# Kernel optimization log

Measured on AMD Instinct MI355X. Metric: run time of the kernel, lower is better.

## Reference

```python
import jax, jax.numpy as jnp
import numpy as np

# ---- static config (matches init_kwargs) ----
B, H, W = 4, 256, 256
TIN, F, P = 10, 4, 8          # time steps in, forecast steps, patch size
CIN = TIN + 2                  # x concatenated with 2-channel grid
E = 768                        # LATENT_DIMS
NB, BS = 8, 96                 # num_blocks, block_size = E // NB
HP, WP = H // P, W // P
MID = 4 * E                    # channel-mixer hidden (MLP_RATIO=4)
DEPTH = 4
LAM = 0.01                     # softshrink sparsity_threshold


def _gelu(t):
    return jax.nn.gelu(t, approximate=False)  # torch default GELU (erf)


def _shrink(t):
    return jnp.sign(t) * jnp.maximum(jnp.abs(t) - LAM, 0.0)


def _spectral(x, w1, b1, w2, b2):
    """SpectralConvBlockDiag: rfft2 -> block-diag complex MLP (GELU) -> softshrink -> irfft2 + residual."""
    bias = x
    b_, h_, w_, c_ = x.shape
    wf = w_ // 2 + 1
    xf = jnp.fft.rfft2(x, axes=(1, 2), norm='ortho').reshape(b_, h_, wf, NB, BS)
    xr, xi = jnp.real(xf), jnp.imag(xf)
    mm = lambda t, w: jnp.einsum('bhfni,nio->bhfno', t, w)
    # complex linear 1 + GELU on real/imag separately
    o1r = _gelu(mm(xr, w1[0]) - mm(xi, w1[1]) + b1[0])
    o1i = _gelu(mm(xi, w1[0]) + mm(xr, w1[1]) + b1[1])
    # complex linear 2 + softshrink
    o2r = _shrink(mm(o1r, w2[0]) - mm(o1i, w2[1]) + b2[0])
    o2i = _shrink(mm(o1i, w2[0]) + mm(o1r, w2[1]) + b2[1])
    xf = (o2r + 1j * o2i).reshape(b_, h_, wf, c_)
    out = jnp.fft.irfft2(xf, s=(h_, w_), axes=(1, 2), norm='ortho')
    return out + bias


def setup_inputs() -> dict:
    key = jax.random.key(0)
    ks = jax.random.split(key, 20)
    s = 0.02
    f32 = jnp.float32
    return {
        'x': jax.random.normal(ks[0], (B, H, W, TIN), f32),
        'grid': jax.random.uniform(ks[1], (B, H, W, 2), f32),
        'conv_w': s * jax.random.normal(ks[2], (E, CIN, P, P), f32),
        'conv_b': s * jax.random.normal(ks[3], (E,), f32),
        'pos_emb': s * jax.random.normal(ks[4], (HP, WP, E), f32),
        'w1': s * jax.random.normal(ks[5], (DEPTH, 2, NB, BS, BS), f32),
        'b1': s * jax.random.normal(ks[6], (DEPTH, 2, NB, BS), f32),
        'w2': s * jax.random.normal(ks[7], (DEPTH, 2, NB, BS, BS), f32),
        'b2': s * jax.random.normal(ks[8], (DEPTH, 2, NB, BS), f32),
        'fc1_w': s * jax.random.normal(ks[9], (DEPTH, E, MID), f32),
        'fc1_b': s * jax.random.normal(ks[10], (DEPTH, MID), f32),
        'fc2_w': s * jax.random.normal(ks[11], (DEPTH, MID, E), f32),
        'fc2_b': s * jax.random.normal(ks[12], (DEPTH, E), f32),
        'head_w1': s * jax.random.normal(ks[13], (E, 2 * E), f32),
        'head_b1': s * jax.random.normal(ks[14], (2 * E,), f32),
        'head_w2': s * jax.random.normal(ks[15], (2 * E, P * P), f32),
        'head_b2': s * jax.random.normal(ks[16], (P * P,), f32),
    }


def reference(x, grid, conv_w, conv_b, pos_emb, w1, b1, w2, b2,
              fc1_w, fc1_b, fc2_w, fc2_b, head_w1, head_b1, head_w2, head_b2):
    # concat grid channels and patch-embed (conv stride==kernel == patch einsum)
    z = jnp.concatenate([x, grid], axis=-1)                  # (B,H,W,CIN)
    patches = z.reshape(B, HP, P, WP, P, CIN)
    t = jnp.einsum('bhpwqc,ecpq->bhwe', patches, conv_w) + conv_b + pos_emb  # (B,HP,WP,E)
    states = []
    for _ in range(F):
        for d in range(DEPTH):                               # AFNOBoundariesBlock (no residual, identity norms)
            t = _spectral(t, w1[d], b1[d], w2[d], b2[d])
            t = _gelu(t @ fc1_w[d] + fc1_b[d]) @ fc2_w[d] + fc2_b[d]
        states.append(t)
    ls = jnp.stack(states, axis=1)                           # (B,F,HP,WP,E)
    h = _gelu(ls @ head_w1 + head_b1) @ head_w2 + head_b2    # (B,F,HP,WP,P*P)
    h = h.reshape(B, F, HP, WP, P, P, 1)
    h = jnp.transpose(h, (0, 6, 2, 4, 3, 5, 1)).reshape(B, 1, H, W, F)
    return jnp.squeeze(h, axis=1)                            # (B,H,W,F)
```

## Files before the change

### kernel.cpp

```cpp
#include <hip/hip_runtime.h>
#include <hip/hip_bf16.h>
#include <math.h>


typedef __attribute__((ext_vector_type(8))) _Float16 half8;
typedef __attribute__((ext_vector_type(4))) _Float16 half4v;
typedef __attribute__((ext_vector_type(4))) float float4v;

__device__ __forceinline__ float gelu_f(float v) {
    return 0.5f * v * (1.0f + erff(v * 0.70710678118654752f));
}
__device__ __forceinline__ float shrink_f(float v) {
    return (v > 0.01f) ? (v - 0.01f) : ((v < -0.01f) ? (v + 0.01f) : 0.0f);
}

#define STEP32 0.19634954084936207f

__device__ __forceinline__ void async16(const void* g, void* l) {
    __builtin_amdgcn_global_load_lds(
        (const __attribute__((address_space(1))) unsigned int*)g,
        (__attribute__((address_space(3))) unsigned int*)l, 16, 0, 0);
}

__global__ __launch_bounds__(256) void gather_patch(const float* __restrict__ x,
        const float* __restrict__ grd, _Float16* __restrict__ A)
{
    int idx = blockIdx.x * 256 + threadIdx.x;
    int j   = idx % 768;
    int tok = idx / 768;
    int c = j >> 6, p = (j >> 3) & 7, q = j & 7;
    int wp = tok & 31, hp = (tok >> 5) & 31, b = tok >> 10;
    int hh = hp * 8 + p, ww = wp * 8 + q;
    float v;
    if (c < 10) v = x[((b * 256 + hh) * 256 + ww) * 10 + c];
    else        v = grd[((b * 256 + hh) * 256 + ww) * 2 + (c - 10)];
    A[idx] = (_Float16)v;
}

__global__ __launch_bounds__(256) void dft_fwd_w(const _Float16* __restrict__ th,
        _Float16* __restrict__ Xr, _Float16* __restrict__ Xi)
{
    __shared__ float2 lut[32];
    int bh = blockIdx.x;
    int tid = threadIdx.x;
    if (tid < 32) { float a = tid * STEP32; lut[tid] = make_float2(cosf(a), sinf(a)); }
    __syncthreads();
    int b = bh >> 5, h = bh & 31;
    int c = blockIdx.y * 256 + tid;
    float v[32];
    #pragma unroll
    for (int w = 0; w < 32; ++w) v[w] = (float)th[(bh * 32 + w) * 768 + c];
    for (int kw = 0; kw <= 16; ++kw) {
        float ar = 0.f, ai = 0.f;
        #pragma unroll
        for (int w = 0; w < 32; ++w) {
            float2 cs = lut[(kw * w) & 31];
            ar += v[w] * cs.x;
            ai -= v[w] * cs.y;
        }
        size_t g = ((size_t)(b * 17 + kw) * 32 + h) * 768 + c;
        Xr[g] = (_Float16)(ar * 0.03125f);
        Xi[g] = (_Float16)(ai * 0.03125f);
    }
}

__global__ __launch_bounds__(256) void dft_inv_w(const _Float16* __restrict__ Yr,
        const _Float16* __restrict__ Yi, _Float16* __restrict__ th)
{
    __shared__ float2 lut[32];
    int bh = blockIdx.x;
    int tid = threadIdx.x;
    if (tid < 32) { float a = tid * STEP32; lut[tid] = make_float2(cosf(a), sinf(a)); }
    __syncthreads();
    int b = bh >> 5, h = bh & 31;
    int c = blockIdx.y * 256 + tid;
    float yr[17], yi[16];
    #pragma unroll
    for (int k = 0; k <= 16; ++k) yr[k] = (float)Yr[((size_t)(b * 17 + k) * 32 + h) * 768 + c];
    #pragma unroll
    for (int k = 1; k <= 15; ++k) yi[k] = (float)Yi[((size_t)(b * 17 + k) * 32 + h) * 768 + c];
    for (int w = 0; w < 32; ++w) {
        float val = yr[0] + ((w & 1) ? -yr[16] : yr[16]);
        #pragma unroll
        for (int k = 1; k <= 15; ++k) {
            float2 cs = lut[(k * w) & 31];
            val += 2.f * (yr[k] * cs.x - yi[k] * cs.y);
        }
        int gi = (bh * 32 + w) * 768 + c;
        th[gi] = (_Float16)(val * 0.03125f + (float)th[gi]);
    }
}

__global__ __launch_bounds__(256) void prep_specw(const float* __restrict__ w1,
        const float* __restrict__ w2, _Float16* __restrict__ out)
{
    __shared__ float tile[96][97];
    int mid = blockIdx.x;
    int n  = mid & 7;
    int ri = (mid >> 3) & 1;
    int l  = (mid >> 4) & 1;
    int d  = mid >> 5;
    const float* src = (l ? w2 : w1) + ((size_t)(d * 2 + ri) * 8 + n) * 9216;
    for (int idx = threadIdx.x; idx < 9216; idx += 256)
        tile[idx / 96][idx % 96] = src[idx];
    __syncthreads();
    _Float16* dst = out + (size_t)mid * 9216;
    for (int idx = threadIdx.x; idx < 9216; idx += 256)
        dst[idx] = (_Float16)tile[idx % 96][idx / 96];
}

__global__ __launch_bounds__(256) void spec_fused(
        _Float16* __restrict__ Xr, _Float16* __restrict__ Xi,
        const _Float16* __restrict__ W1r, const _Float16* __restrict__ W1i,
        const _Float16* __restrict__ W2r, const _Float16* __restrict__ W2i,
        const float* __restrict__ b1r, const float* __restrict__ b1i,
        const float* __restrict__ b2r, const float* __restrict__ b2i)
{
    __shared__ alignas(16) _Float16 Ec[1024], Es[1024];
    __shared__ alignas(16) _Float16 XTr[3840], XTi[3840];
    __shared__ alignas(16) _Float16 Zr[3328], Zi[3328];
    __shared__ alignas(16) _Float16 Sr[3328], Si[3328];

    const int bk = blockIdx.x;
    const int n  = blockIdx.y;
    const int tid = threadIdx.x;
    const int wave = tid >> 6, lane = tid & 63;
    const int wr = wave >> 1, wc = wave & 1;
    const int lr = lane & 15, quad = lane >> 4;
    const size_t base = (size_t)bk * 24576 + n * 96;

    for (int i = tid; i < 1024; i += 256) {
        int kh = i >> 5, h = i & 31;
        float a = ((kh * h) & 31) * STEP32;
        Ec[i] = (_Float16)cosf(a);
        Es[i] = (_Float16)sinf(a);
    }
    for (int i = tid; i < 384; i += 256) {
        int h = i / 12, cc = (i % 12) * 8;
        half8 vr = *(const half8*)(Xr + base + (size_t)h * 768 + cc);
        half8 vi = *(const half8*)(Xi + base + (size_t)h * 768 + cc);
        #pragma unroll
        for (int e = 0; e < 8; ++e) {
            XTr[(cc + e) * 40 + h] = vr[e];
            XTi[(cc + e) * 40 + h] = vi[e];
        }
    }
    __syncthreads();

    const _Float16* w1r = W1r + (size_t)n * 9216;
    const _Float16* w1i = W1i + (size_t)n * 9216;
    const _Float16* w2r = W2r + (size_t)n * 9216;
    const _Float16* w2i = W2i + (size_t)n * 9216;

    half8 eC = *(const half8*)&Ec[(wr * 16 + lr) * 32 + quad * 8];
    half8 eS = *(const half8*)&Es[(wr * 16 + lr) * 32 + quad * 8];
    half8 eSn = -eS;

    {
        float4v zr[3], zi[3];
        #pragma unroll
        for (int j = 0; j < 3; ++j) { float4v z = {0,0,0,0}; zr[j] = z; zi[j] = z; }
        #pragma unroll
        for (int j = 0; j < 3; ++j) {
            int c = wc * 48 + j * 16 + lr;
            half8 xr = *(const half8*)&XTr[c * 40 + quad * 8];
            half8 xi = *(const half8*)&XTi[c * 40 + quad * 8];
            zr[j] = __builtin_amdgcn_mfma_f32_16x16x32_f16(eC,  xr, zr[j], 0, 0, 0);
            zr[j] = __builtin_amdgcn_mfma_f32_16x16x32_f16(eS,  xi, zr[j], 0, 0, 0);
            zi[j] = __builtin_amdgcn_mfma_f32_16x16x32_f16(eC,  xi, zi[j], 0, 0, 0);
            zi[j] = __builtin_amdgcn_mfma_f32_16x16x32_f16(eSn, xr, zi[j], 0, 0, 0);
        }
        #pragma unroll
        for (int j = 0; j < 3; ++j) {
            int c = wc * 48 + j * 16 + lr;
            #pragma unroll
            for (int r = 0; r < 4; ++r) {
                int kh = wr * 16 + quad * 4 + r;
                Zr[kh * 104 + c] = (_Float16)zr[j][r];
                Zi[kh * 104 + c] = (_Float16)zi[j][r];
            }
        }
    }
    __syncthreads();

    {
        float4v sr[3], si[3];
        #pragma unroll
        for (int j = 0; j < 3; ++j) { float4v z = {0,0,0,0}; sr[j] = z; si[j] = z; }
        #pragma unroll
        for (int kc = 0; kc < 3; ++kc) {
            half8 ar = *(const half8*)&Zr[(wr * 16 + lr) * 104 + kc * 32 + quad * 8];
            half8 ai = *(const half8*)&Zi[(wr * 16 + lr) * 104 + kc * 32 + quad * 8];
            half8 ain = -ai;
            #pragma unroll
            for (int j = 0; j < 3; ++j) {
                int o = wc * 48 + j * 16 + lr;
                half8 br = *(const half8*)&w1r[o * 96 + kc * 32 + quad * 8];
                half8 bi = *(const half8*)&w1i[o * 96 + kc * 32 + quad * 8];
                sr[j] = __builtin_amdgcn_mfma_f32_16x16x32_f16(ar,  br, sr[j], 0, 0, 0);
                sr[j] = __builtin_amdgcn_mfma_f32_16x16x32_f16(ain, bi, sr[j], 0, 0, 0);
                si[j] = __builtin_amdgcn_mfma_f32_16x16x32_f16(ai,  br, si[j], 0, 0, 0);
                si[j] = __builtin_amdgcn_mfma_f32_16x16x32_f16(ar,  bi, si[j], 0, 0, 0);
            }
        }
        #pragma unroll
        for (int j = 0; j < 3; ++j) {
            int o = wc * 48 + j * 16 + lr;
            float br = b1r[n * 96 + o], bi = b1i[n * 96 + o];
            #pragma unroll
            for (int r = 0; r < 4; ++r) {
                int kh = wr * 16 + quad * 4 + r;
                Sr[kh * 104 + o] = (_Float16)gelu_f(sr[j][r] + br);
                Si[kh * 104 + o] = (_Float16)gelu_f(si[j][r] + bi);
            }
        }
    }
    __syncthreads();

    {
        float4v tr[3], ti[3];
        #pragma unroll
        for (int j = 0; j < 3; ++j) { float4v z = {0,0,0,0}; tr[j] = z; ti[j] = z; }
        #pragma unroll
        for (int kc = 0; kc < 3; ++kc) {
            half8 ar = *(const half8*)&Sr[(wr * 16 + lr) * 104 + kc * 32 + quad * 8];
            half8 ai = *(const half8*)&Si[(wr * 16 + lr) * 104 + kc * 32 + quad * 8];
            half8 ain = -ai;
            #pragma unroll
            for (int j = 0; j < 3; ++j) {
                int o = wc * 48 + j * 16 + lr;
                half8 br = *(const half8*)&w2r[o * 96 + kc * 32 + quad * 8];
                half8 bi = *(const half8*)&w2i[o * 96 + kc * 32 + quad * 8];
                tr[j] = __builtin_amdgcn_mfma_f32_16x16x32_f16(ar,  br, tr[j], 0, 0, 0);
                tr[j] = __builtin_amdgcn_mfma_f32_16x16x32_f16(ain, bi, tr[j], 0, 0, 0);
                ti[j] = __builtin_amdgcn_mfma_f32_16x16x32_f16(ai,  br, ti[j], 0, 0, 0);
                ti[j] = __builtin_amdgcn_mfma_f32_16x16x32_f16(ar,  bi, ti[j], 0, 0, 0);
            }
        }
        #pragma unroll
        for (int j = 0; j < 3; ++j) {
            int o = wc * 48 + j * 16 + lr;
            float br = b2r[n * 96 + o], bi = b2i[n * 96 + o];
            #pragma unroll
            for (int r = 0; r < 4; ++r) {
                int kh = wr * 16 + quad * 4 + r;
                XTr[o * 40 + kh] = (_Float16)shrink_f(tr[j][r] + br);
                XTi[o * 40 + kh] = (_Float16)shrink_f(ti[j][r] + bi);
            }
        }
    }
    __syncthreads();

    {
        float4v yr[3], yi[3];
        #pragma unroll
        for (int j = 0; j < 3; ++j) { float4v z = {0,0,0,0}; yr[j] = z; yi[j] = z; }
        #pragma unroll
        for (int j = 0; j < 3; ++j) {
            int c = wc * 48 + j * 16 + lr;
            half8 t2r = *(const half8*)&XTr[c * 40 + quad * 8];
            half8 t2i = *(const half8*)&XTi[c * 40 + quad * 8];
            yr[j] = __builtin_amdgcn_mfma_f32_16x16x32_f16(eC,  t2r, yr[j], 0, 0, 0);
            yr[j] = __builtin_amdgcn_mfma_f32_16x16x32_f16(eSn, t2i, yr[j], 0, 0, 0);
            yi[j] = __builtin_amdgcn_mfma_f32_16x16x32_f16(eC,  t2i, yi[j], 0, 0, 0);
            yi[j] = __builtin_amdgcn_mfma_f32_16x16x32_f16(eS,  t2r, yi[j], 0, 0, 0);
        }
        #pragma unroll
        for (int j = 0; j < 3; ++j) {
            int c = wc * 48 + j * 16 + lr;
            #pragma unroll
            for (int r = 0; r < 4; ++r) {
                int h = wr * 16 + quad * 4 + r;
                Zr[h * 104 + c] = (_Float16)yr[j][r];
                Zi[h * 104 + c] = (_Float16)yi[j][r];
            }
        }
    }
    __syncthreads();

    for (int i = tid; i < 384; i += 256) {
        int h = i / 12, cc = (i % 12) * 8;
        half8 vr = *(const half8*)&Zr[h * 104 + cc];
        half8 vi = *(const half8*)&Zi[h * 104 + cc];
        *(half8*)(Xr + base + (size_t)h * 768 + cc) = vr;
        *(half8*)(Xi + base + (size_t)h * 768 + cc) = vi;
    }
}

__global__ __launch_bounds__(256) void cvt_f16(const float* __restrict__ in,
        _Float16* __restrict__ out)
{
    int i = blockIdx.x * 256 + threadIdx.x;
    float4 v = ((const float4*)in)[i];
    half4v o;
    o.x = (_Float16)v.x; o.y = (_Float16)v.y; o.z = (_Float16)v.z; o.w = (_Float16)v.w;
    ((half4v*)out)[i] = o;
}

__global__ __launch_bounds__(256) void cvt_transpose(const float* __restrict__ in,
        _Float16* __restrict__ out, int K, int N)
{
    __shared__ float tile[32][33];
    int kb = blockIdx.x * 32, nb = blockIdx.y * 32;
    int tx = threadIdx.x & 31, ty = threadIdx.x >> 5;
    #pragma unroll
    for (int r = 0; r < 32; r += 8)
        tile[ty + r][tx] = in[(size_t)(kb + ty + r) * N + nb + tx];
    __syncthreads();
    #pragma unroll
    for (int r = 0; r < 32; r += 8)
        out[(size_t)(nb + ty + r) * K + kb + tx] = (_Float16)tile[tx][ty + r];
}

template<int BN, int ACT>
__global__ __launch_bounds__(512, 4) void gemm128d(const _Float16* __restrict__ A,
        const _Float16* __restrict__ Bt, const float* __restrict__ bias,
        _Float16* __restrict__ C16, int M, int N, int K)
{
    constexpr int WN  = BN / 4;
    constexpr int FN  = WN / 16;
    constexpr int AU  = 2;
    constexpr int BU  = BN / 64;
    constexpr int LPT = AU + BU;
    __shared__ _Float16 Al[2][128 * 64];
    __shared__ _Float16 Bl[2][BN * 64];

    const int tid  = threadIdx.x;
    const int wave = tid >> 6;
    const int lane = tid & 63;
    const int wr   = wave >> 2;
    const int wc   = wave & 3;
    const int lr   = lane & 15;
    const int quad = lane >> 4;

    const int gx = gridDim.x, gy = gridDim.y, nbk = gx * gy;
    int bx = blockIdx.x, by = blockIdx.y;
    if (!(gy & 3) && !(gx & 1)) {
        int id = by * gx + bx;
        int xcd = id & 7, j = id >> 3;
        int cols = gx >> 1;
        int rows = gy >> 2;
        int jr = j / cols, jc = j % cols;
        by = (xcd >> 1) * rows + jr;
        bx = (xcd & 1) * cols + jc;
    } else if (!(nbk & 7)) {
        int id  = by * gx + bx;
        int id2 = (id & 7) * (nbk >> 3) + (id >> 3);
        by = id2 / gx; bx = id2 % gx;
    }
    const int row0 = by * 128;
    const int col0 = bx * BN;

    const int srow = lane >> 3;
    const int schk = (lane & 7) ^ (srow & 7);
    const _Float16* Ab = A  + (size_t)(row0 + wave * 8 + srow) * K + schk * 8;
    const _Float16* Bb = Bt + (size_t)(col0 + wave * 8 + srow) * K + schk * 8;

    auto stage = [&](int b, int kt) {
        const int k0 = kt * 64;
        #pragma unroll
        for (int u = 0; u < AU; ++u)
            async16(Ab + (size_t)u * 64 * K + k0, &Al[b][(u * 64 + wave * 8) * 64]);
        #pragma unroll
        for (int u = 0; u < BU; ++u)
            async16(Bb + (size_t)u * 64 * K + k0, &Bl[b][(u * 64 + wave * 8) * 64]);
    };

    float4v acc[4][FN];
    #pragma unroll
    for (int m = 0; m < 4; ++m)
        #pragma unroll
        for (int n = 0; n < FN; ++n) {
            float4v z = {0.f, 0.f, 0.f, 0.f};
            acc[m][n] = z;
        }

    auto compute = [&](int cb) {
        #pragma unroll
        for (int ks = 0; ks < 2; ++ks) {
            const int cA = ((ks * 4 + quad) ^ (lr & 7)) * 8;
            half8 bf[FN];
            #pragma unroll
            for (int n = 0; n < FN; ++n)
                bf[n] = *(const half8*)&Bl[cb][(wc * WN + n * 16 + lr) * 64 + cA];
            half8 af[4];
            #pragma unroll
            for (int m = 0; m < 4; ++m)
                af[m] = *(const half8*)&Al[cb][(wr * 64 + m * 16 + lr) * 64 + cA];
            __builtin_amdgcn_s_setprio(1);
            #pragma unroll
            for (int m = 0; m < 4; ++m)
                #pragma unroll
                for (int n = 0; n < FN; ++n)
                    acc[m][n] = __builtin_amdgcn_mfma_f32_16x16x32_f16(af[m], bf[n], acc[m][n], 0, 0, 0);
            __builtin_amdgcn_s_setprio(0);
        }
    };

    const int NT = K >> 6;
    stage(0, 0);
    stage(1, 1);
    for (int t = 0; t < NT; ++t) {
        if (t + 1 < NT) asm volatile("s_waitcnt vmcnt(5)" ::: "memory");
        else            asm volatile("s_waitcnt vmcnt(0)" ::: "memory");
        __builtin_amdgcn_s_barrier();
        compute(t & 1);
        __builtin_amdgcn_s_barrier();
        if (t + 2 < NT) stage(t & 1, t + 2);
    }

    #pragma unroll
    for (int n = 0; n < FN; ++n) {
        int col = col0 + wc * WN + n * 16 + lr;
        float bj = bias[col];
        #pragma unroll
        for (int m = 0; m < 4; ++m) {
            int row = row0 + wr * 64 + m * 16 + quad * 4;
            #pragma unroll
            for (int r = 0; r < 4; ++r) {
                float v = acc[m][n][r] + bj;
                if (ACT) v = gelu_f(v);
                C16[(size_t)(row + r) * N + col] = (_Float16)v;
            }
        }
    }
}

__global__ __launch_bounds__(256, 2) void fc2_fused(const _Float16* __restrict__ A,
        const _Float16* __restrict__ Bt, const float* __restrict__ bias,
        _Float16* __restrict__ C16, _Float16* __restrict__ XR,
        _Float16* __restrict__ XI)
{
    constexpr int K = 3072;
    constexpr int NT = 48;
    __shared__ _Float16 Al[2][64 * 64];
    __shared__ _Float16 Bl[2][96 * 64];
    __shared__ alignas(16) _Float16 Tl[2 * 96 * 40];
    __shared__ alignas(16) _Float16 ECl[1024], ESl[1024];

    const int tid  = threadIdx.x;
    const int wave = tid >> 6;
    const int lane = tid & 63;
    const int wr   = wave >> 1;
    const int wc   = wave & 1;
    const int lr   = lane & 15;
    const int quad = lane >> 4;

    for (int i = tid; i < 1024; i += 256) {
        int kw = i >> 5, w = i & 31;
        float a = ((kw * w) & 31) * STEP32;
        ECl[i] = (_Float16)(cosf(a) * 0.03125f);
        ESl[i] = (_Float16)(-sinf(a) * 0.03125f);
    }

    const int gx = gridDim.x, gy = gridDim.y;
    int bx = blockIdx.x, by = blockIdx.y;
    {
        int id = by * gx + bx;
        int xcd = id & 7, j = id >> 3;
        int cols = gx >> 1;
        int rows = gy >> 2;
        int jr = j / cols, jc = j % cols;
        by = (xcd >> 1) * rows + jr;
        bx = (xcd & 1) * cols + jc;
    }
    const int row0 = by * 64;
    const int col0 = bx * 96;

    const int srow = lane >> 3;
    const int schk = (lane & 7) ^ srow;
    const _Float16* Ab = A  + (size_t)(row0 + wave * 8 + srow) * K + schk * 8;
    const _Float16* Bb = Bt + (size_t)(col0 + wave * 8 + srow) * K + schk * 8;

    auto stage = [&](int b, int kt) {
        const int k0 = kt * 64;
        #pragma unroll
        for (int u = 0; u < 2; ++u)
            async16(Ab + (size_t)u * 32 * K + k0, &Al[b][(u * 32 + wave * 8) * 64]);
        #pragma unroll
        for (int u = 0; u < 3; ++u)
            async16(Bb + (size_t)u * 32 * K + k0, &Bl[b][(u * 32 + wave * 8) * 64]);
    };

    float4v acc[2][3];
    #pragma unroll
    for (int m = 0; m < 2; ++m)
        #pragma unroll
        for (int n = 0; n < 3; ++n) {
            float4v z = {0.f, 0.f, 0.f, 0.f};
            acc[m][n] = z;
        }

    auto compute = [&](int cb) {
        #pragma unroll
        for (int ks = 0; ks < 2; ++ks) {
            const int cA = ((ks * 4 + quad) ^ (lr & 7)) * 8;
            half8 bf[3];
            #pragma unroll
            for (int n = 0; n < 3; ++n)
                bf[n] = *(const half8*)&Bl[cb][(wc * 48 + n * 16 + lr) * 64 + cA];
            half8 af[2];
            #pragma unroll
            for (int m = 0; m < 2; ++m)
                af[m] = *(const half8*)&Al[cb][(wr * 32 + m * 16 + lr) * 64 + cA];
            __builtin_amdgcn_s_setprio(1);
            #pragma unroll
            for (int m = 0; m < 2; ++m)
                #pragma unroll
                for (int n = 0; n < 3; ++n)
                    acc[m][n] = __builtin_amdgcn_mfma_f32_16x16x32_f16(af[m], bf[n], acc[m][n], 0, 0, 0);
            __builtin_amdgcn_s_setprio(0);
        }
    };

    stage(0, 0);
    stage(1, 1);
    for (int t = 0; t < NT; ++t) {
        if (t + 1 < NT) asm volatile("s_waitcnt vmcnt(5)" ::: "memory");
        else            asm volatile("s_waitcnt vmcnt(0)" ::: "memory");
        __builtin_amdgcn_s_barrier();
        compute(t & 1);
        __builtin_amdgcn_s_barrier();
        if (t + 2 < NT) stage(t & 1, t + 2);
    }

    #pragma unroll
    for (int n = 0; n < 3; ++n) {
        int cc  = wc * 48 + n * 16 + lr;
        int col = col0 + cc;
        float bj = bias[col];
        #pragma unroll
        for (int m = 0; m < 2; ++m) {
            int row = row0 + wr * 32 + m * 16 + quad * 4;
            #pragma unroll
            for (int r = 0; r < 4; ++r) {
                float v = acc[m][n][r] + bj;
                C16[(size_t)(row + r) * 768 + col] = (_Float16)v;
                int lrow = row + r - row0;
                Tl[((lrow >> 5) * 96 + cc) * 40 + (lrow & 31)] = (_Float16)v;
            }
        }
    }
    __syncthreads();

    const int h     = wave >> 1;
    const int cbase = (wave & 1) * 48;
    const int b     = row0 >> 10;
    const int hp    = ((row0 >> 5) & 31) + h;
    half8 eC0 = *(const half8*)&ECl[lr * 32 + quad * 8];
    half8 eC1 = *(const half8*)&ECl[(16 + lr) * 32 + quad * 8];
    half8 eS0 = *(const half8*)&ESl[lr * 32 + quad * 8];
    half8 eS1 = *(const half8*)&ESl[(16 + lr) * 32 + quad * 8];
    float4v xr[2][3], xi[2][3];
    #pragma unroll
    for (int m = 0; m < 2; ++m)
        #pragma unroll
        for (int nj = 0; nj < 3; ++nj) {
            float4v z = {0.f, 0.f, 0.f, 0.f};
            xr[m][nj] = z; xi[m][nj] = z;
        }
    #pragma unroll
    for (int nj = 0; nj < 3; ++nj) {
        half8 tb = *(const half8*)&Tl[(h * 96 + cbase + nj * 16 + lr) * 40 + quad * 8];
        xr[0][nj] = __builtin_amdgcn_mfma_f32_16x16x32_f16(eC0, tb, xr[0][nj], 0, 0, 0);
        xr[1][nj] = __builtin_amdgcn_mfma_f32_16x16x32_f16(eC1, tb, xr[1][nj], 0, 0, 0);
        xi[0][nj] = __builtin_amdgcn_mfma_f32_16x16x32_f16(eS0, tb, xi[0][nj], 0, 0, 0);
        xi[1][nj] = __builtin_amdgcn_mfma_f32_16x16x32_f16(eS1, tb, xi[1][nj], 0, 0, 0);
    }
    #pragma unroll
    for (int m = 0; m < 2; ++m)
        #pragma unroll
        for (int r = 0; r < 4; ++r) {
            int kw = m * 16 + quad * 4 + r;
            if (kw < 17) {
                #pragma unroll
                for (int nj = 0; nj < 3; ++nj) {
                    int c = col0 + cbase + nj * 16 + lr;
                    size_t g = ((size_t)(b * 17 + kw) * 32 + hp) * 768 + c;
                    XR[g] = (_Float16)xr[m][nj][r];
                    XI[g] = (_Float16)xi[m][nj][r];
                }
            }
        }
}

__global__ __launch_bounds__(256, 4) void head2_k(const _Float16* __restrict__ A,
        const _Float16* __restrict__ Bt, const float* __restrict__ bias,
        float* __restrict__ C32, int f_idx)
{
    constexpr int K = 1536;
    constexpr int NT = 24;
    __shared__ _Float16 Al[2][64 * 64];
    __shared__ _Float16 Bl[2][64 * 64];

    const int tid  = threadIdx.x;
    const int wave = tid >> 6;
    const int lane = tid & 63;
    const int wr   = wave >> 1;
    const int wc   = wave & 1;
    const int lr   = lane & 15;
    const int quad = lane >> 4;

    const int row0 = blockIdx.x * 64;

    const int srow = lane >> 3;
    const int schk = (lane & 7) ^ srow;
    const _Float16* Ab = A  + (size_t)(row0 + wave * 8 + srow) * K + schk * 8;
    const _Float16* Bb = Bt + (size_t)(wave * 8 + srow) * K + schk * 8;

    auto stage = [&](int b, int kt) {
        const int k0 = kt * 64;
        #pragma unroll
        for (int u = 0; u < 2; ++u)
            async16(Ab + (size_t)u * 32 * K + k0, &Al[b][(u * 32 + wave * 8) * 64]);
        #pragma unroll
        for (int u = 0; u < 2; ++u)
            async16(Bb + (size_t)u * 32 * K + k0, &Bl[b][(u * 32 + wave * 8) * 64]);
    };

    float4v acc[2][2];
    #pragma unroll
    for (int m = 0; m < 2; ++m)
        #pragma unroll
        for (int n = 0; n < 2; ++n) {
            float4v z = {0.f, 0.f, 0.f, 0.f};
            acc[m][n] = z;
        }

    auto compute = [&](int cb) {
        #pragma unroll
        for (int ks = 0; ks < 2; ++ks) {
            const int cA = ((ks * 4 + quad) ^ (lr & 7)) * 8;
            half8 bf[2], af[2];
            #pragma unroll
            for (int n = 0; n < 2; ++n)
                bf[n] = *(const half8*)&Bl[cb][(wc * 32 + n * 16 + lr) * 64 + cA];
            #pragma unroll
            for (int m = 0; m < 2; ++m)
                af[m] = *(const half8*)&Al[cb][(wr * 32 + m * 16 + lr) * 64 + cA];
            #pragma unroll
            for (int m = 0; m < 2; ++m)
                #pragma unroll
                for (int n = 0; n < 2; ++n)
                    acc[m][n] = __builtin_amdgcn_mfma_f32_16x16x32_f16(af[m], bf[n], acc[m][n], 0, 0, 0);
        }
    };

    stage(0, 0);
    stage(1, 1);
    for (int t = 0; t < NT; ++t) {
        if (t + 1 < NT) asm volatile("s_waitcnt vmcnt(4)" ::: "memory");
        else            asm volatile("s_waitcnt vmcnt(0)" ::: "memory");
        __builtin_amdgcn_s_barrier();
        compute(t & 1);
        __builtin_amdgcn_s_barrier();
        if (t + 2 < NT) stage(t & 1, t + 2);
    }

    #pragma unroll
    for (int n = 0; n < 2; ++n) {
        int col = wc * 32 + n * 16 + lr;
        float bj = bias[col];
        int p = col >> 3, q = col & 7;
        #pragma unroll
        for (int m = 0; m < 2; ++m) {
            int row = row0 + wr * 32 + m * 16 + quad * 4;
            #pragma unroll
            for (int r = 0; r < 4; ++r) {
                float v = acc[m][n][r] + bj;
                int rowv = row + r;
                int bq = rowv >> 10, hp = (rowv >> 5) & 31, wp = rowv & 31;
                C32[(((size_t)(bq * 256 + hp * 8 + p)) * 256 + wp * 8 + q) * 4 + f_idx] = v;
            }
        }
    }
}

template<int BN, int OUT_MODE, int ACT>
__global__ __launch_bounds__(256) void gemm_h(const _Float16* __restrict__ A,
        const _Float16* __restrict__ Bt, const float* __restrict__ bias,
        const float* __restrict__ pos, float* __restrict__ C32,
        _Float16* __restrict__ C16, _Float16* __restrict__ XR,
        _Float16* __restrict__ XI, int M, int N, int K, int f_idx)
{
    constexpr int WN  = BN / 2;
    constexpr int FN  = WN / 16;
    constexpr int NBJ = BN / 64;
    constexpr int LPT = 2 + NBJ;
    __shared__ _Float16 Al[4][128 * 32];
    __shared__ _Float16 Bl[4][BN * 32];

    const int tid  = threadIdx.x;
    const int wave = tid >> 6;
    const int lane = tid & 63;
    const int wr   = wave >> 1;
    const int wc   = wave & 1;
    const int lr   = lane & 15;
    const int quad = lane >> 4;

    const int gx = gridDim.x, gy = gridDim.y, nbk = gx * gy;
    int bx = blockIdx.x, by = blockIdx.y;
    if (!(gy & 3) && !(gx & 1)) {
        int id = by * gx + bx;
        int xcd = id & 7, j = id >> 3;
        int cols = gx >> 1;
        int rows = gy >> 2;
        int jr = j / cols, jc = j % cols;
        by = (xcd >> 1) * rows + jr;
        bx = (xcd & 1) * cols + jc;
    } else if (!(nbk & 7)) {
        int id  = by * gx + bx;
        int id2 = (id & 7) * (nbk >> 3) + (id >> 3);
        by = id2 / gx; bx = id2 % gx;
    }
    const int row0 = by * 128;
    const int col0 = bx * BN;

    const int srow = lane >> 2;
    const int skof = ((lane & 3) ^ (srow & 3)) * 8;

    auto stage = [&](int b, int kt) {
        const int k0 = kt << 5;
        #pragma unroll
        for (int j = 0; j < 2; ++j)
            async16(A + (size_t)(row0 + j * 64 + wave * 16 + srow) * K + k0 + skof,
                    &Al[b][(j * 64 + wave * 16) * 32]);
        #pragma unroll
        for (int j = 0; j < NBJ; ++j)
            async16(Bt + (size_t)(col0 + j * 64 + wave * 16 + srow) * K + k0 + skof,
                    &Bl[b][(j * 64 + wave * 16) * 32]);
    };

    float4v acc[4][FN];
    #pragma unroll
    for (int i = 0; i < 4; ++i)
        #pragma unroll
        for (int j = 0; j < FN; ++j) {
            float4v z = {0.f, 0.f, 0.f, 0.f};
            acc[i][j] = z;
        }

    auto compute = [&](int cb) {
        const int cA = (quad ^ (lr & 3)) * 8;
        half8 af[4], bf[FN];
        #pragma unroll
        for (int i = 0; i < 4; ++i)
            af[i] = *(const half8*)&Al[cb][(wr * 64 + i * 16 + lr) * 32 + cA];
        #pragma unroll
        for (int j = 0; j < FN; ++j)
            bf[j] = *(const half8*)&Bl[cb][(wc * WN + j * 16 + lr) * 32 + cA];
        #pragma unroll
        for (int i = 0; i < 4; ++i)
            #pragma unroll
            for (int j = 0; j < FN; ++j)
                acc[i][j] = __builtin_amdgcn_mfma_f32_16x16x32_f16(af[i], bf[j], acc[i][j], 0, 0, 0);
    };

    const int KT = K >> 5;
    stage(0, 0); stage(1, 1); stage(2, 2);
    int kt = 0;
    for (; kt < KT - 3; ++kt) {
        stage((kt + 3) & 3, kt + 3);
        if constexpr (LPT == 4) asm volatile("s_waitcnt vmcnt(12)" ::: "memory");
        else                    asm volatile("s_waitcnt vmcnt(9)"  ::: "memory");
        __builtin_amdgcn_s_barrier();
        compute(kt & 3);
        asm volatile("" ::: "memory");
        __builtin_amdgcn_s_barrier();
    }
    if constexpr (LPT == 4) asm volatile("s_waitcnt vmcnt(8)" ::: "memory");
    else                    asm volatile("s_waitcnt vmcnt(6)" ::: "memory");
    __builtin_amdgcn_s_barrier();
    compute(kt & 3); ++kt;
    asm volatile("" ::: "memory");
    __builtin_amdgcn_s_barrier();
    if constexpr (LPT == 4) asm volatile("s_waitcnt vmcnt(4)" ::: "memory");
    else                    asm volatile("s_waitcnt vmcnt(3)" ::: "memory");
    __builtin_amdgcn_s_barrier();
    compute(kt & 3); ++kt;
    asm volatile("" ::: "memory");
    __builtin_amdgcn_s_barrier();
    asm volatile("s_waitcnt vmcnt(0)" ::: "memory");
    __builtin_amdgcn_s_barrier();
    compute(kt & 3);

    #pragma unroll
    for (int j = 0; j < FN; ++j) {
        int col = col0 + wc * WN + j * 16 + lr;
        float bj = bias[col];
        #pragma unroll
        for (int i = 0; i < 4; ++i) {
            int row = row0 + wr * 64 + i * 16 + quad * 4;
            #pragma unroll
            for (int r = 0; r < 4; ++r) {
                float v = acc[i][j][r] + bj;
                if (pos) v += pos[(size_t)((row + r) & 1023) * N + col];
                if (ACT) v = gelu_f(v);
                if (OUT_MODE == 3) {
                    int rowv = row + r;
                    int bq = rowv >> 10, hp = (rowv >> 5) & 31, wp = rowv & 31;
                    int p = col >> 3, q = col & 7;
                    C32[(((size_t)(bq * 256 + hp * 8 + p)) * 256 + wp * 8 + q) * 4 + f_idx] = v;
                } else {
                    C16[(size_t)(row + r) * N + col] = (_Float16)v;
                }
            }
        }
    }
}

extern "C" void kernel_launch(void* const* d_in, const int* in_sizes, int n_in,
                              void* d_out, int out_size, void* d_ws, size_t ws_size,
                              hipStream_t stream) {
    const float* x        = (const float*)d_in[0];
    const float* grd      = (const float*)d_in[1];
    const float* conv_w   = (const float*)d_in[2];
    const float* conv_b   = (const float*)d_in[3];
    const float* pos_emb  = (const float*)d_in[4];
    const float* w1       = (const float*)d_in[5];
    const float* b1       = (const float*)d_in[6];
    const float* w2       = (const float*)d_in[7];
    const float* b2       = (const float*)d_in[8];
    const float* fc1_w    = (const float*)d_in[9];
    const float* fc1_b    = (const float*)d_in[10];
    const float* fc2_w    = (const float*)d_in[11];
    const float* fc2_b    = (const float*)d_in[12];
    const float* head_w1  = (const float*)d_in[13];
    const float* head_b1  = (const float*)d_in[14];
    const float* head_w2  = (const float*)d_in[15];
    const float* head_b2  = (const float*)d_in[16];
    float* out = (float*)d_out;
    float* ws  = (float*)d_ws;

    float* pf = ws;
    _Float16* t_h     = (_Float16*)pf; pf += 1572864;
    _Float16* Wsp     = (_Float16*)pf; pf += 589824;
    _Float16* h1t     = (_Float16*)pf; pf += 589824;
    _Float16* h2t     = (_Float16*)pf; pf += 49152;
    _Float16* convw_h = (_Float16*)pf; pf += 294912;
    float* alias    = pf;              pf += 6291456;
    _Float16* hid_h = (_Float16*)alias;
    _Float16* WtAll = (_Float16*)pf;   pf += 9437184;
    _Float16* xa_r_fb = (_Float16*)alias;
    _Float16* xa_i_fb = (_Float16*)(alias + 835584);
    _Float16* xa_r_fu = (_Float16*)pf;
    _Float16* xa_i_fu = (_Float16*)(pf + 835584);
    size_t full_total = (size_t)(pf - ws) + 1671168;
    bool full = ws_size >= full_total * 4ull;
    _Float16* xa_r = full ? xa_r_fu : xa_r_fb;
    _Float16* xa_i = full ? xa_i_fu : xa_i_fb;
    _Float16* A_h  = (_Float16*)alias;

    prep_specw<<<dim3(128), 256, 0, stream>>>(w1, w2, Wsp);
    cvt_f16<<<dim3(576), 256, 0, stream>>>(conv_w, convw_h);
    cvt_transpose<<<dim3(24, 48), 256, 0, stream>>>(head_w1, h1t, 768, 1536);
    cvt_transpose<<<dim3(48, 2), 256, 0, stream>>>(head_w2, h2t, 1536, 64);
    for (int d = 0; d < 4; ++d) {
        cvt_transpose<<<dim3(24, 96), 256, 0, stream>>>(
            fc1_w + (size_t)d * 2359296, WtAll + (size_t)(2 * d) * 2359296, 768, 3072);
        cvt_transpose<<<dim3(96, 24), 256, 0, stream>>>(
            fc2_w + (size_t)d * 2359296, WtAll + (size_t)(2 * d + 1) * 2359296, 3072, 768);
    }
    gather_patch<<<dim3(12288), 256, 0, stream>>>(x, grd, A_h);
    gemm_h<128, 1, 0><<<dim3(6, 32), 256, 0, stream>>>(
        A_h, convw_h, conv_b, pos_emb, nullptr, t_h, nullptr, nullptr, 4096, 768, 768, 0);
    dft_fwd_w<<<dim3(128, 3), 256, 0, stream>>>(t_h, xa_r, xa_i);

    for (int f = 0; f < 4; ++f) {
        for (int d = 0; d < 4; ++d) {
            spec_fused<<<dim3(68, 8), 256, 0, stream>>>(
                xa_r, xa_i,
                Wsp + (size_t)(d * 4 + 0) * 73728, Wsp + (size_t)(d * 4 + 1) * 73728,
                Wsp + (size_t)(d * 4 + 2) * 73728, Wsp + (size_t)(d * 4 + 3) * 73728,
                b1 + d * 1536, b1 + d * 1536 + 768,
                b2 + d * 1536, b2 + d * 1536 + 768);
            dft_inv_w<<<dim3(128, 3), 256, 0, stream>>>(xa_r, xa_i, t_h);
            gemm128d<192, 1><<<dim3(16, 32), 512, 0, stream>>>(
                t_h, WtAll + (size_t)(2 * d) * 2359296, fc1_b + d * 3072,
                hid_h, 4096, 3072, 768);
            if (full) {
                fc2_fused<<<dim3(8, 64), 256, 0, stream>>>(
                    hid_h, WtAll + (size_t)(2 * d + 1) * 2359296, fc2_b + d * 768,
                    t_h, xa_r, xa_i);
            } else {
                gemm_h<64, 1, 0><<<dim3(12, 32), 256, 0, stream>>>(
                    hid_h, WtAll + (size_t)(2 * d + 1) * 2359296, fc2_b + d * 768,
                    nullptr, nullptr, t_h, nullptr, nullptr, 4096, 768, 3072, 0);
                dft_fwd_w<<<dim3(128, 3), 256, 0, stream>>>(t_h, xa_r, xa_i);
            }
        }
        gemm128d<192, 1><<<dim3(8, 32), 512, 0, stream>>>(
            t_h, h1t, head_b1, hid_h, 4096, 1536, 768);
        head2_k<<<dim3(64), 256, 0, stream>>>(
            hid_h, h2t, head_b2, out, f);
    }
}
```

Baseline: 2.024 ms.

## Compute inverse W-direction DFT with MFMA instead of scalar loops

Replaces the scalar inverse real DFT along W with a small matrix multiply on MFMA units. The twiddle matrix (with Hermitian weights and normalization) is built in LDS, the frequency coefficients are transposed into LDS, and each wave computes a 32x48 output tile with one K=32 MFMA per 16x16 tile before adding the residual. This removes the per-thread scalar FMA loops, at the cost of fp16 twiddle precision and an LDS transpose with a swizzled scatter.

```diff
diff --git a/kernel.cpp b/kernel.cpp
--- a/kernel.cpp
+++ b/kernel.cpp
@@ -64,31 +64,80 @@
     }
 }
 
-__global__ __launch_bounds__(256) void dft_inv_w(const _Float16* __restrict__ Yr,
+__global__ __launch_bounds__(256) void idft_w_mfma(const _Float16* __restrict__ Yr,
         const _Float16* __restrict__ Yi, _Float16* __restrict__ th)
 {
-    __shared__ float2 lut[32];
-    int bh = blockIdx.x;
-    int tid = threadIdx.x;
-    if (tid < 32) { float a = tid * STEP32; lut[tid] = make_float2(cosf(a), sinf(a)); }
+    __shared__ alignas(16) _Float16 Yt[192 * 40];
+    __shared__ alignas(16) _Float16 El[32 * 40];
+
+    const int tid  = threadIdx.x;
+    const int wave = tid >> 6;
+    const int lane = tid & 63;
+    const int lr   = lane & 15;
+    const int quad = lane >> 4;
+
+    const int bh = blockIdx.x;
+    const int b  = bh >> 5, h = bh & 31;
+    const int c0 = blockIdx.y * 192;
+
+    for (int i = tid; i < 1024; i += 256) {
+        int w = i >> 5, s = i & 31;
+        float val;
+        if (s <= 16) {
+            float g = (s == 0 || s == 16) ? 1.f : 2.f;
+            val = g * cosf(((w * s) & 31) * STEP32) * 0.03125f;
+        } else {
+            int k = s - 16;
+            val = -2.f * sinf(((w * k) & 31) * STEP32) * 0.03125f;
+        }
+        El[w * 40 + s] = (_Float16)val;
+    }
+
+    #pragma unroll
+    for (int i = 0; i < 3; ++i) {
+        int u    = tid + i * 256;
+        int slot = u / 24;
+        int cg   = u % 24;
+        const _Float16* src;
+        if (slot < 17) src = Yr + ((size_t)(b * 17 + slot) * 32 + h) * 768;
+        else           src = Yi + ((size_t)(b * 17 + (slot - 16)) * 32 + h) * 768;
+        half8 v = *(const half8*)(src + c0 + cg * 8);
+        #pragma unroll
+        for (int e = 0; e < 8; ++e) {
+            int el = e ^ (cg & 7);
+            Yt[(cg * 8 + el) * 40 + slot] = v[el];
+        }
+    }
     __syncthreads();
-    int b = bh >> 5, h = bh & 31;
-    int c = blockIdx.y * 256 + tid;
-    float yr[17], yi[16];
-    #pragma unroll
-    for (int k = 0; k <= 16; ++k) yr[k] = (float)Yr[((size_t)(b * 17 + k) * 32 + h) * 768 + c];
-    #pragma unroll
-    for (int k = 1; k <= 15; ++k) yi[k] = (float)Yi[((size_t)(b * 17 + k) * 32 + h) * 768 + c];
-    for (int w = 0; w < 32; ++w) {
-        float val = yr[0] + ((w & 1) ? -yr[16] : yr[16]);
-        #pragma unroll
-        for (int k = 1; k <= 15; ++k) {
-            float2 cs = lut[(k * w) & 31];
-            val += 2.f * (yr[k] * cs.x - yi[k] * cs.y);
-        }
-        int gi = (bh * 32 + w) * 768 + c;
-        th[gi] = (_Float16)(val * 0.03125f + (float)th[gi]);
-    }
+
+    half8 af[2], bf[3];
+    #pragma unroll
+    for (int m = 0; m < 2; ++m)
+        af[m] = *(const half8*)&El[(m * 16 + lr) * 40 + quad * 8];
+    #pragma unroll
+    for (int n = 0; n < 3; ++n)
+        bf[n] = *(const half8*)&Yt[(wave * 48 + n * 16 + lr) * 40 + quad * 8];
+    float4v acc[2][3];
+    #pragma unroll
+    for (int m = 0; m < 2; ++m)
+        #pragma unroll
+        for (int n = 0; n < 3; ++n) {
+            float4v z = {0.f, 0.f, 0.f, 0.f};
+            acc[m][n] = __builtin_amdgcn_mfma_f32_16x16x32_f16(af[m], bf[n], z, 0, 0, 0);
+        }
+
+    #pragma unroll
+    for (int m = 0; m < 2; ++m)
+        #pragma unroll
+        for (int n = 0; n < 3; ++n) {
+            int c = c0 + wave * 48 + n * 16 + lr;
+            #pragma unroll
+            for (int r = 0; r < 4; ++r) {
+                int w = m * 16 + quad * 4 + r;
+                size_t gi = (size_t)(bh * 32 + w) * 768 + c;
+                th[gi] = (_Float16)(acc[m][n][r] + (float)th[gi]);
+            }
+        }
 }
 
 __global__ __launch_bounds__(256) void prep_specw(const float* __restrict__ w1,
@@ -874,7 +923,7 @@
                 Wsp + (size_t)(d * 4 + 2) * 73728, Wsp + (size_t)(d * 4 + 3) * 73728,
                 b1 + d * 1536, b1 + d * 1536 + 768,
                 b2 + d * 1536, b2 + d * 1536 + 768);
-            dft_inv_w<<<dim3(128, 3), 256, 0, stream>>>(xa_r, xa_i, t_h);
+            idft_w_mfma<<<dim3(128, 4), 256, 0, stream>>>(xa_r, xa_i, t_h);
             gemm128d<192, 1><<<dim3(16, 32), 512, 0, stream>>>(
                 t_h, WtAll + (size_t)(2 * d) * 2359296, fc1_b + d * 3072,
                 hid_h, 4096, 3072, 768);
```

Result: faster. 1.755 ms (-13.3%).
